# Kernel tuning notes

Measured on AMD Instinct MI355X. Metric: run time of the kernel, lower is better.

The kernel has to match this reference:

```python
import jax, jax.numpy as jnp
import numpy as np

NUM_CLUSTERS = 64
DIM = 128
ALPHA = 100.0


def setup_inputs() -> dict:
    key = jax.random.key(0)
    k1, k2 = jax.random.split(key)
    x = jax.random.normal(k1, (32, 4096, DIM), dtype=jnp.float32)
    centroids = jax.random.uniform(k2, (NUM_CLUSTERS, DIM), dtype=jnp.float32)
    return {"x": x, "centroids": centroids}


def reference(x, centroids):
    # x: [B, N, D], centroids: [K, D]
    # Euclidean distances (torch.cdist p=2): [B, N, K]
    x2 = jnp.sum(x * x, axis=-1, keepdims=True)            # [B, N, 1]
    c2 = jnp.sum(centroids * centroids, axis=-1)            # [K]
    xc = jnp.einsum('bnd,kd->bnk', x, centroids)            # [B, N, K]
    dist2 = jnp.maximum(x2 + c2[None, None, :] - 2.0 * xc, 0.0)
    distances = jnp.sqrt(dist2)
    soft_assign = jax.nn.softmax(-ALPHA * distances, axis=2)  # [B, N, K]
    # vlad[b,k,:] = sum_n a[b,n,k] * (x[b,n,:] - c[k,:])
    vlad = jnp.einsum('bnk,bnd->bkd', soft_assign, x) \
         - jnp.sum(soft_assign, axis=1)[:, :, None] * centroids[None, :, :]
    B = x.shape[0]
    vlad = vlad.reshape(B, -1)
    # F.normalize(p=2, dim=1) with default eps=1e-12
    norm = jnp.maximum(jnp.linalg.norm(vlad, axis=1, keepdims=True), 1e-12)
    return vlad / norm
```

## Files before the change

kernel.cpp:

```cpp
#include <hip/hip_runtime.h>

typedef _Float16 half8 __attribute__((ext_vector_type(8)));
typedef _Float16 half4_t __attribute__((ext_vector_type(4)));
typedef float floatx4 __attribute__((ext_vector_type(4)));

static constexpr int NB  = 32;
static constexpr int NP  = 4096;
static constexpr int DD  = 128;
static constexpr int KC  = 64;
static constexpr int TN  = 64;
static constexpr int TPB = 4;
static constexpr int SXP = 136;
static constexpr int STP = 72;

#define ALPHA_  100.0f
#define LOG2E_  1.44269504088896f

__global__ __launch_bounds__(256, 2)
void vlad_phase1(const float* __restrict__ xg, const float* __restrict__ cg,
                 float* __restrict__ vlad, float* __restrict__ colsum)
{
    __shared__ __align__(16) _Float16 sx[TN][SXP];
    __shared__ __align__(16) _Float16 sxt[DD][STP];
    __shared__ __align__(16) _Float16 sat[KC][STP];
    __shared__ __align__(16) _Float16 sclo[KC][SXP];
    __shared__ float sx2[TN];
    __shared__ float sc2[KC];

    const int tid  = threadIdx.x;
    const int lane = tid & 63;
    const int w    = tid >> 6;
    const int l15  = lane & 15;
    const int quad = lane >> 4;
    const int b    = blockIdx.y;
    const float* xb = xg + (size_t)b * NP * DD;

    half8 chi[4][4];
#pragma unroll
    for (int mt = 0; mt < 4; ++mt)
#pragma unroll
        for (int ks = 0; ks < 4; ++ks) {
            const float* p = cg + (mt*16 + l15)*DD + ks*32 + quad*8;
            float4 a  = *(const float4*)p;
            float4 bb = *(const float4*)(p + 4);
            half8 h;
            h[0]=(_Float16)a.x;  h[1]=(_Float16)a.y;  h[2]=(_Float16)a.z;  h[3]=(_Float16)a.w;
            h[4]=(_Float16)bb.x; h[5]=(_Float16)bb.y; h[6]=(_Float16)bb.z; h[7]=(_Float16)bb.w;
            chi[mt][ks] = h;
        }
    {
        int k = tid >> 2, qq = tid & 3;
        const float* rp = cg + k*DD + qq*32;
        float c2p = 0.f;
#pragma unroll
        for (int j = 0; j < 8; ++j) {
            float4 v = *(const float4*)(rp + j*4);
            c2p += v.x*v.x + v.y*v.y + v.z*v.z + v.w*v.w;
            half4_t lo;
            lo[0] = (_Float16)(v.x - (float)(_Float16)v.x);
            lo[1] = (_Float16)(v.y - (float)(_Float16)v.y);
            lo[2] = (_Float16)(v.z - (float)(_Float16)v.z);
            lo[3] = (_Float16)(v.w - (float)(_Float16)v.w);
            *(half4_t*)&sclo[k][(qq*8 + j)*4] = lo;
        }
        c2p += __shfl_xor(c2p, 1);
        c2p += __shfl_xor(c2p, 2);
        if (qq == 0) sc2[k] = c2p;
    }

    floatx4 acc2[8];
#pragma unroll
    for (int i = 0; i < 8; ++i) acc2[i] = (floatx4){0.f, 0.f, 0.f, 0.f};
    float csreg[4][4];
#pragma unroll
    for (int mt = 0; mt < 4; ++mt)
#pragma unroll
        for (int r = 0; r < 4; ++r) csreg[mt][r] = 0.f;

    for (int tt = 0; tt < TPB; ++tt) {
        const int n0 = (blockIdx.x * TPB + tt) * TN;

#pragma unroll
        for (int i = 0; i < 4; ++i) {
            int u = i*256 + tid;
            int n = u >> 4, d8 = u & 15;
            const float* p = xb + (size_t)(n0 + n)*DD + d8*8;
            float4 a  = *(const float4*)p;
            float4 bb = *(const float4*)(p + 4);
            half8 h;
            h[0]=(_Float16)a.x;  h[1]=(_Float16)a.y;  h[2]=(_Float16)a.z;  h[3]=(_Float16)a.w;
            h[4]=(_Float16)bb.x; h[5]=(_Float16)bb.y; h[6]=(_Float16)bb.z; h[7]=(_Float16)bb.w;
            *(half8*)&sx[n][d8*8] = h;
            float s = a.x*a.x + a.y*a.y + a.z*a.z + a.w*a.w
                    + bb.x*bb.x + bb.y*bb.y + bb.z*bb.z + bb.w*bb.w;
            s += __shfl_xor(s, 1); s += __shfl_xor(s, 2);
            s += __shfl_xor(s, 4); s += __shfl_xor(s, 8);
            if ((lane & 15) == 0) sx2[n] = s;
        }
        __syncthreads();

        floatx4 acc1[4];
#pragma unroll
        for (int mt = 0; mt < 4; ++mt) acc1[mt] = (floatx4){0.f, 0.f, 0.f, 0.f};
#pragma unroll
        for (int ks = 0; ks < 4; ++ks) {
            half8 xf = *(const half8*)&sx[w*16 + l15][ks*32 + quad*8];
#pragma unroll
            for (int mt = 0; mt < 4; ++mt) {
                half8 cl = *(const half8*)&sclo[mt*16 + l15][ks*32 + quad*8];
                acc1[mt] = __builtin_amdgcn_mfma_f32_16x16x32_f16(chi[mt][ks], xf, acc1[mt], 0, 0, 0);
                acc1[mt] = __builtin_amdgcn_mfma_f32_16x16x32_f16(cl,          xf, acc1[mt], 0, 0, 0);
            }
        }

        const int n_loc = w*16 + l15;
        float x2v = sx2[n_loc];
        float dist[4][4];
#pragma unroll
        for (int mt = 0; mt < 4; ++mt) {
            floatx4 c2v = *(const floatx4*)&sc2[mt*16 + quad*4];
#pragma unroll
            for (int r = 0; r < 4; ++r) {
                float d2 = x2v + c2v[r] - 2.f*acc1[mt][r];
                dist[mt][r] = sqrtf(fmaxf(d2, 0.f));
            }
        }
        float dmin = dist[0][0];
#pragma unroll
        for (int mt = 0; mt < 4; ++mt)
#pragma unroll
            for (int r = 0; r < 4; ++r) dmin = fminf(dmin, dist[mt][r]);
        dmin = fminf(dmin, __shfl_xor(dmin, 16));
        dmin = fminf(dmin, __shfl_xor(dmin, 32));
        float pv[4][4];
        float psum = 0.f;
#pragma unroll
        for (int mt = 0; mt < 4; ++mt)
#pragma unroll
            for (int r = 0; r < 4; ++r) {
                float e = exp2f((dmin - dist[mt][r]) * (ALPHA_ * LOG2E_));
                pv[mt][r] = e; psum += e;
            }
        psum += __shfl_xor(psum, 16);
        psum += __shfl_xor(psum, 32);
        float invs = 1.0f / psum;
#pragma unroll
        for (int mt = 0; mt < 4; ++mt)
#pragma unroll
            for (int r = 0; r < 4; ++r) {
                float a = pv[mt][r] * invs;
                csreg[mt][r] += a;
                sat[mt*16 + quad*4 + r][n_loc] = (_Float16)a;
            }

        {
            const int l5  = lane & 31;
            const int nn  = 2 * l5;
            const int dhi = (lane >> 5) * 16;
#pragma unroll
            for (int j = 0; j < 4; ++j) {
                int d4 = (w + 4*j + dhi) * 4;
                ushort4 lo = *(const ushort4*)&sx[nn][d4];
                ushort4 hi = *(const ushort4*)&sx[nn + 1][d4];
                *(unsigned*)&sxt[d4 + 0][nn] = (unsigned)lo.x | ((unsigned)hi.x << 16);
                *(unsigned*)&sxt[d4 + 1][nn] = (unsigned)lo.y | ((unsigned)hi.y << 16);
                *(unsigned*)&sxt[d4 + 2][nn] = (unsigned)lo.z | ((unsigned)hi.z << 16);
                *(unsigned*)&sxt[d4 + 3][nn] = (unsigned)lo.w | ((unsigned)hi.w << 16);
            }
        }
        __syncthreads();

#pragma unroll
        for (int ks = 0; ks < 2; ++ks) {
            half8 af = *(const half8*)&sat[w*16 + l15][ks*32 + quad*8];
#pragma unroll
            for (int nt = 0; nt < 8; ++nt) {
                half8 bf = *(const half8*)&sxt[nt*16 + l15][ks*32 + quad*8];
                acc2[nt] = __builtin_amdgcn_mfma_f32_16x16x32_f16(af, bf, acc2[nt], 0, 0, 0);
            }
        }
    }

#pragma unroll
    for (int mt = 0; mt < 4; ++mt)
#pragma unroll
        for (int r = 0; r < 4; ++r) {
            float cs = csreg[mt][r];
            cs += __shfl_xor(cs, 1); cs += __shfl_xor(cs, 2);
            cs += __shfl_xor(cs, 4); cs += __shfl_xor(cs, 8);
            if (l15 == 0) atomicAdd(&colsum[b*KC + mt*16 + quad*4 + r], cs);
        }

#pragma unroll
    for (int nt = 0; nt < 8; ++nt)
#pragma unroll
        for (int r = 0; r < 4; ++r) {
            int k = w*16 + quad*4 + r;
            int d = nt*16 + l15;
            atomicAdd(&vlad[((size_t)b*KC + k)*DD + d], acc2[nt][r]);
        }
}

__global__ __launch_bounds__(256)
void vlad_finalize(const float* __restrict__ vlad, const float* __restrict__ colsum,
                   const float* __restrict__ cg, float* __restrict__ out)
{
    __shared__ float red[4];
    const int b = blockIdx.x;
    const int tid = threadIdx.x;
    float v[32];
    float ss = 0.f;
#pragma unroll
    for (int i = 0; i < 32; ++i) {
        int idx = i*256 + tid;
        float val = vlad[(size_t)b*8192 + idx] - colsum[b*64 + (idx >> 7)] * cg[idx];
        v[i] = val;
        ss += val * val;
    }
#pragma unroll
    for (int m = 1; m < 64; m <<= 1) ss += __shfl_xor(ss, m);
    if ((tid & 63) == 0) red[tid >> 6] = ss;
    __syncthreads();
    float tot = red[0] + red[1] + red[2] + red[3];
    float scale = 1.0f / fmaxf(sqrtf(tot), 1e-12f);
#pragma unroll
    for (int i = 0; i < 32; ++i)
        out[(size_t)b*8192 + i*256 + tid] = v[i] * scale;
}

extern "C" void kernel_launch(void* const* d_in, const int* in_sizes, int n_in,
                              void* d_out, int out_size, void* d_ws, size_t ws_size,
                              hipStream_t stream)
{
    (void)in_sizes; (void)n_in; (void)out_size; (void)ws_size;
    const float* x = (const float*)d_in[0];
    const float* c = (const float*)d_in[1];
    float* out  = (float*)d_out;
    float* vlad = (float*)d_ws;
    float* cs   = vlad + (size_t)NB*KC*DD;

    hipMemsetAsync(d_ws, 0, (size_t)(NB*KC*DD + NB*KC) * sizeof(float), stream);
    vlad_phase1<<<dim3(16, 32), 256, 0, stream>>>(x, c, vlad, cs);
    vlad_finalize<<<32, 256, 0, stream>>>(vlad, cs, c, out);
}
```

Before: 135.7 us.

## Load x directly into MFMA fragments, drop staging tile, compute colsum via MFMA

Each lane now loads its own x row slice straight from global memory into registers, converts it to fp16 for the distance MFMA, and writes it transposed into an XOR-swizzled shared tile. This removes the row-major x staging buffer, the separate transpose pass and one barrier per tile. Row norms are reduced with lane shuffles, and the per-cluster assignment sums are produced by an extra MFMA against a ones vector in place of register accumulation plus shuffle reductions. The launch bound is raised to 3 blocks per CU because shared memory use drops. In exchange, global loads become less coalesced (each lane reads scattered 32-byte chunks), a trailing barrier is added per tile, and register pressure is tighter.

```diff
diff --git a/kernel.cpp b/kernel.cpp
--- a/kernel.cpp
+++ b/kernel.cpp
@@ -10,21 +10,19 @@
 static constexpr int KC  = 64;
 static constexpr int TN  = 64;
 static constexpr int TPB = 4;
-static constexpr int SXP = 136;
+static constexpr int SCP = 136;
 static constexpr int STP = 72;
 
 #define ALPHA_  100.0f
 #define LOG2E_  1.44269504088896f
 
-__global__ __launch_bounds__(256, 2)
+__global__ __launch_bounds__(256, 3)
 void vlad_phase1(const float* __restrict__ xg, const float* __restrict__ cg,
                  float* __restrict__ vlad, float* __restrict__ colsum)
 {
-    __shared__ __align__(16) _Float16 sx[TN][SXP];
     __shared__ __align__(16) _Float16 sxt[DD][STP];
     __shared__ __align__(16) _Float16 sat[KC][STP];
-    __shared__ __align__(16) _Float16 sclo[KC][SXP];
-    __shared__ float sx2[TN];
+    __shared__ __align__(16) _Float16 sclo[KC][SCP];
     __shared__ float sc2[KC];
 
     const int tid  = threadIdx.x;
@@ -67,44 +65,48 @@
         c2p += __shfl_xor(c2p, 2);
         if (qq == 0) sc2[k] = c2p;
     }
+    __syncthreads();
 
     floatx4 acc2[8];
 #pragma unroll
     for (int i = 0; i < 8; ++i) acc2[i] = (floatx4){0.f, 0.f, 0.f, 0.f};
-    float csreg[4][4];
-#pragma unroll
-    for (int mt = 0; mt < 4; ++mt)
-#pragma unroll
-        for (int r = 0; r < 4; ++r) csreg[mt][r] = 0.f;
+    floatx4 accs = (floatx4){0.f, 0.f, 0.f, 0.f};
+
+    half8 onesf;
+#pragma unroll
+    for (int j = 0; j < 8; ++j) onesf[j] = (_Float16)((l15 == 0) ? 1.0f : 0.0f);
+
+    const int nloc = w*16 + l15;
+    const int scol = nloc ^ (quad << 4);
 
     for (int tt = 0; tt < TPB; ++tt) {
         const int n0 = (blockIdx.x * TPB + tt) * TN;
-
-#pragma unroll
-        for (int i = 0; i < 4; ++i) {
-            int u = i*256 + tid;
-            int n = u >> 4, d8 = u & 15;
-            const float* p = xb + (size_t)(n0 + n)*DD + d8*8;
-            float4 a  = *(const float4*)p;
-            float4 bb = *(const float4*)(p + 4);
-            half8 h;
-            h[0]=(_Float16)a.x;  h[1]=(_Float16)a.y;  h[2]=(_Float16)a.z;  h[3]=(_Float16)a.w;
-            h[4]=(_Float16)bb.x; h[5]=(_Float16)bb.y; h[6]=(_Float16)bb.z; h[7]=(_Float16)bb.w;
-            *(half8*)&sx[n][d8*8] = h;
-            float s = a.x*a.x + a.y*a.y + a.z*a.z + a.w*a.w
-                    + bb.x*bb.x + bb.y*bb.y + bb.z*bb.z + bb.w*bb.w;
-            s += __shfl_xor(s, 1); s += __shfl_xor(s, 2);
-            s += __shfl_xor(s, 4); s += __shfl_xor(s, 8);
-            if ((lane & 15) == 0) sx2[n] = s;
-        }
-        __syncthreads();
-
+        const float* xrow = xb + (size_t)(n0 + nloc) * DD + quad*8;
+
+        float4 fa[4], fb[4];
+#pragma unroll
+        for (int ks = 0; ks < 4; ++ks) {
+            fa[ks] = *(const float4*)(xrow + ks*32);
+            fb[ks] = *(const float4*)(xrow + ks*32 + 4);
+        }
+
+        float ssq = 0.f;
         floatx4 acc1[4];
 #pragma unroll
         for (int mt = 0; mt < 4; ++mt) acc1[mt] = (floatx4){0.f, 0.f, 0.f, 0.f};
+
 #pragma unroll
         for (int ks = 0; ks < 4; ++ks) {
-            half8 xf = *(const half8*)&sx[w*16 + l15][ks*32 + quad*8];
+            half8 xf;
+            xf[0]=(_Float16)fa[ks].x; xf[1]=(_Float16)fa[ks].y;
+            xf[2]=(_Float16)fa[ks].z; xf[3]=(_Float16)fa[ks].w;
+            xf[4]=(_Float16)fb[ks].x; xf[5]=(_Float16)fb[ks].y;
+            xf[6]=(_Float16)fb[ks].z; xf[7]=(_Float16)fb[ks].w;
+            ssq += fa[ks].x*fa[ks].x + fa[ks].y*fa[ks].y + fa[ks].z*fa[ks].z + fa[ks].w*fa[ks].w
+                 + fb[ks].x*fb[ks].x + fb[ks].y*fb[ks].y + fb[ks].z*fb[ks].z + fb[ks].w*fb[ks].w;
+#pragma unroll
+            for (int j = 0; j < 8; ++j)
+                sxt[ks*32 + quad*8 + j][scol] = xf[j];
 #pragma unroll
             for (int mt = 0; mt < 4; ++mt) {
                 half8 cl = *(const half8*)&sclo[mt*16 + l15][ks*32 + quad*8];
@@ -112,16 +114,16 @@
                 acc1[mt] = __builtin_amdgcn_mfma_f32_16x16x32_f16(cl,          xf, acc1[mt], 0, 0, 0);
             }
         }
-
-        const int n_loc = w*16 + l15;
-        float x2v = sx2[n_loc];
+        ssq += __shfl_xor(ssq, 16);
+        ssq += __shfl_xor(ssq, 32);
+
         float dist[4][4];
 #pragma unroll
         for (int mt = 0; mt < 4; ++mt) {
             floatx4 c2v = *(const floatx4*)&sc2[mt*16 + quad*4];
 #pragma unroll
             for (int r = 0; r < 4; ++r) {
-                float d2 = x2v + c2v[r] - 2.f*acc1[mt][r];
+                float d2 = ssq + c2v[r] - 2.f*acc1[mt][r];
                 dist[mt][r] = sqrtf(fmaxf(d2, 0.f));
             }
         }
@@ -148,48 +150,24 @@
         for (int mt = 0; mt < 4; ++mt)
 #pragma unroll
             for (int r = 0; r < 4; ++r) {
-                float a = pv[mt][r] * invs;
-                csreg[mt][r] += a;
-                sat[mt*16 + quad*4 + r][n_loc] = (_Float16)a;
-            }
-
-        {
-            const int l5  = lane & 31;
-            const int nn  = 2 * l5;
-            const int dhi = (lane >> 5) * 16;
-#pragma unroll
-            for (int j = 0; j < 4; ++j) {
-                int d4 = (w + 4*j + dhi) * 4;
-                ushort4 lo = *(const ushort4*)&sx[nn][d4];
-                ushort4 hi = *(const ushort4*)&sx[nn + 1][d4];
-                *(unsigned*)&sxt[d4 + 0][nn] = (unsigned)lo.x | ((unsigned)hi.x << 16);
-                *(unsigned*)&sxt[d4 + 1][nn] = (unsigned)lo.y | ((unsigned)hi.y << 16);
-                *(unsigned*)&sxt[d4 + 2][nn] = (unsigned)lo.z | ((unsigned)hi.z << 16);
-                *(unsigned*)&sxt[d4 + 3][nn] = (unsigned)lo.w | ((unsigned)hi.w << 16);
-            }
-        }
+                sat[mt*16 + quad*4 + r][scol] = (_Float16)(pv[mt][r] * invs);
+            }
         __syncthreads();
 
 #pragma unroll
-        for (int ks = 0; ks < 2; ++ks) {
-            half8 af = *(const half8*)&sat[w*16 + l15][ks*32 + quad*8];
+        for (int ks2 = 0; ks2 < 2; ++ks2) {
+            const int nbase = ks2*32 + quad*8;
+            half8 af = *(const half8*)&sat[w*16 + l15][nbase ^ ((l15 >> 2) << 4)];
+            accs = __builtin_amdgcn_mfma_f32_16x16x32_f16(af, onesf, accs, 0, 0, 0);
 #pragma unroll
             for (int nt = 0; nt < 8; ++nt) {
-                half8 bf = *(const half8*)&sxt[nt*16 + l15][ks*32 + quad*8];
+                const int d = nt*16 + l15;
+                half8 bf = *(const half8*)&sxt[d][nbase ^ (((d >> 3) & 3) << 4)];
                 acc2[nt] = __builtin_amdgcn_mfma_f32_16x16x32_f16(af, bf, acc2[nt], 0, 0, 0);
             }
         }
-    }
-
-#pragma unroll
-    for (int mt = 0; mt < 4; ++mt)
-#pragma unroll
-        for (int r = 0; r < 4; ++r) {
-            float cs = csreg[mt][r];
-            cs += __shfl_xor(cs, 1); cs += __shfl_xor(cs, 2);
-            cs += __shfl_xor(cs, 4); cs += __shfl_xor(cs, 8);
-            if (l15 == 0) atomicAdd(&colsum[b*KC + mt*16 + quad*4 + r], cs);
-        }
+        __syncthreads();
+    }
 
 #pragma unroll
     for (int nt = 0; nt < 8; ++nt)
@@ -199,6 +177,11 @@
             int d = nt*16 + l15;
             atomicAdd(&vlad[((size_t)b*KC + k)*DD + d], acc2[nt][r]);
         }
+    if (l15 == 0) {
+#pragma unroll
+        for (int r = 0; r < 4; ++r)
+            atomicAdd(&colsum[b*KC + w*16 + quad*4 + r], accs[r]);
+    }
 }
 
 __global__ __launch_bounds__(256)
```

Measured after the change: 128.8 us. 5.1% less time.
